# Optimization experiments

Hardware: AMD Instinct MI355X
Metric: run time of the kernel (lower is better)

Reference implementation:

```python
import jax, jax.numpy as jnp
import numpy as np

SAMPLES = 1024
LAM = 0.00051
IOR = 1.515
T_PROP = 8.74
CA = 0.9
LENSLET_CA = 0.165
RMIN = 5.5 * (IOR - 1.0)
RMAX = 29.0 * (IOR - 1.0)
NZ = 10
NLENS = 29
TAU = 30.0
LSE_P = 0.01
PS = 3.6 / SAMPLES
K = 2.0 * np.pi / LAM


def _grids():
    xg = np.linspace(-1.8, 1.8, SAMPLES).astype(np.float32)
    xgm, ygm = np.meshgrid(xg, xg)
    fx = np.linspace(-1.0 / (2.0 * PS), 1.0 / (2.0 * PS), SAMPLES).astype(np.float32)
    Fx, Fy = np.meshgrid(fx, fx)
    return xgm, ygm, Fx, Fy


def _bessj1(x):
    # Numerical Recipes rational approximation of J1 (numpy, setup-time only)
    ax = np.abs(x)
    y = x * x
    p1 = x * (72362614232.0 + y * (-7895059235.0 + y * (242396853.1 + y * (-2972611.439 + y * (15704.48260 + y * (-30.16036606))))))
    q1 = 144725228442.0 + y * (2300535178.0 + y * (18583304.74 + y * (99447.43394 + y * (376.9991397 + y))))
    small = p1 / q1
    axs = np.maximum(ax, 1e-12)
    z = 8.0 / axs
    y2 = z * z
    xx = axs - 2.356194491
    p2 = 1.0 + y2 * (0.183105e-2 + y2 * (-0.3516396496e-4 + y2 * (0.2457520174e-5 + y2 * (-0.240337019e-6))))
    q2 = 0.04687499995 + y2 * (-0.2002690873e-3 + y2 * (0.8449199096e-5 + y2 * (-0.88228987e-6 + y2 * 0.105787412e-6)))
    big = np.sqrt(0.636619772 / axs) * (np.cos(xx) * p2 - z * np.sin(xx) * q2) * np.sign(x)
    return np.where(ax < 8.0, small, big)


def _target_and_mask():
    xgm, ygm, _, _ = _grids()
    target_res = 0.005 * 6  # target_res * M
    D = 1.22 * LAM / np.sin(2.0 * np.arctan(target_res / (2.0 * T_PROP)))
    xa = K * D * np.sin(np.arctan(xgm / T_PROP)) / 2.0
    ya = K * D * np.sin(np.arctan(ygm / T_PROP)) / 2.0
    Ra = np.sqrt(xa * xa + ya * ya)
    ta = (2.0 * _bessj1(Ra) / Ra) ** 2
    ta = ta / np.sqrt(np.sum(ta ** 2))
    tF = np.abs(np.fft.fft2(np.fft.fftshift(ta))) ** 2
    dcm = np.ones_like(tF)
    dcm[:3, :3] = 0; dcm[-2:, :1] = 0; dcm[:1, -2:] = 0; dcm[-2:, -2:] = 0
    dc_mask = ((dcm * tF) > 1e-3 * tF.max()).astype(np.float32)
    return tF.astype(np.float32), dc_mask


def setup_inputs() -> dict:
    rng = np.random.default_rng(0)
    rlist = rng.permutation(1.0 / np.linspace(1.0 / RMAX, 1.0 / RMIN, NLENS)).astype(np.float32)
    th = rng.uniform(0.0, 2.0 * np.pi, NLENS)
    rad = (CA - LENSLET_CA) * np.sqrt(rng.uniform(0.0, 1.0, NLENS))
    xpos = (rad * np.cos(th)).astype(np.float32)
    ypos = (rad * np.sin(th)).astype(np.float32)
    zmin_v = 1.0 / (1.0 / T_PROP - 1.0 / 5.5)
    zmax_v = 1.0 / (1.0 / T_PROP - 1.0 / 29.0)
    defocus = (1.0 / np.linspace(1.0 / zmin_v, 1.0 / zmax_v, NZ)).astype(np.float32)
    tF, dc_mask = _target_and_mask()
    return {
        'rlist': jnp.asarray(rlist), 'xpos': jnp.asarray(xpos), 'ypos': jnp.asarray(ypos),
        'defocus_list': jnp.asarray(defocus),
        'target_F': jnp.asarray(tF), 'dc_mask': jnp.asarray(dc_mask),
    }


def reference(rlist, xpos, ypos, defocus_list, target_F, dc_mask):
    xgm_np, ygm_np, Fx_np, Fy_np = _grids()
    xgm, ygm = jnp.asarray(xgm_np), jnp.asarray(ygm_np)
    Fx, Fy = jnp.asarray(Fx_np), jnp.asarray(Fy_np)

    # ---- lenslet surface synthesis (irregular per-lenslet scatter) ----
    dx2 = (xgm[None] - xpos[:, None, None]) ** 2 + (ygm[None] - ypos[:, None, None]) ** 2  # [N,H,W]
    in_lens = dx2 <= LENSLET_CA ** 2
    r = rlist[:, None, None]
    r2_safe = jnp.where(in_lens, dx2, 0.0)  # avoid nan grads outside lenslet
    sag = r - jnp.sqrt(jnp.maximum(r * r - r2_safe, 1e-12))  # plano-convex sag
    Tsurf = jnp.sum(jnp.where(in_lens, sag, 0.0), axis=0)  # [H,W]
    aper = ((jnp.sum(in_lens.astype(jnp.float32), axis=0) > 0) & (xgm ** 2 + ygm ** 2 <= CA ** 2)).astype(jnp.float32)
    phi_lens = (K * (IOR - 1.0)) * Tsurf

    # ---- angular-spectrum propagation kernel over distance t ----
    kz = jnp.sqrt(jnp.maximum((1.0 / LAM) ** 2 - Fx ** 2 - Fy ** 2, 0.0))
    H = jnp.fft.ifftshift(jnp.exp(1j * (2.0 * np.pi * T_PROP) * kz))

    def psf_one(z):
        phi_in = K * (xgm ** 2 + ygm ** 2) / (2.0 * z)  # paraxial defocus from virtual plane z
        U1 = aper * jnp.exp(1j * (phi_in + phi_lens))
        U2 = jnp.fft.ifft2(jnp.fft.fft2(U1) * H)
        p = jnp.abs(U2) ** 2
        return p / jnp.sum(p)  # l1 psf normalization

    zstack = jax.vmap(psf_one)(defocus_list)  # [Nz,H,W]

    # ---- stack spectrum ----
    S = jnp.fft.fft2(jnp.fft.fftshift(zstack, axes=(-2, -1)))  # [Nz,H,W] complex
    normsize = float(SAMPLES * SAMPLES)

    # diagonal terms: |S|^2 vs target autocorrelation spectrum, dc-masked
    diag = jnp.sum(dc_mask[None] * jnp.square((jnp.abs(S) ** 2 - target_F[None]) / normsize), axis=(-2, -1))  # [Nz]

    # off-diagonal terms: log-sum-exp of |cross-correlation|
    i1, i2 = np.triu_indices(NZ, k=1)  # 45 fixed pairs
    Fcorr = jnp.conj(S[i1]) * S[i2]  # [45,H,W]
    ccorr = jnp.abs(jnp.fft.ifft2(Fcorr))
    off = (TAU * LSE_P) * jax.scipy.special.logsumexp(ccorr.reshape(len(i1), -1) / LSE_P, axis=-1)  # [45]

    return jnp.concatenate([diag, off], axis=0)  # [55]
```

## Files before the change

### kernel.cpp

```cpp
#include <hip/hip_runtime.h>
#include <math.h>

#define NSMP 1024
#define NZ 10
#define NLENS 29
#define NPAIR 45
#define NUNIT 23
#define UBATCH 4
#define CPB 4
#define CSTR 1028

static __device__ __forceinline__ float2 cmulf(float2 a, float2 b){
    return make_float2(a.x*b.x - a.y*b.y, a.x*b.y + a.y*b.x);
}
#define SW(i) ((i) ^ (((i)>>5)&31))

static constexpr double PI2   = 6.283185307179586;
static constexpr double KD    = PI2/0.00051;
static constexpr double F0D   = 1.0/(2.0*(3.6/1024.0));
static constexpr double FSTEP = 2.0*F0D/1023.0;
static constexpr double IL2D  = (1.0/0.00051)*(1.0/0.00051);
static constexpr double TPPID = PI2*8.74;

static __device__ __forceinline__ void fill_W(float2* W, int tid, int nthr){
    for (int t = tid; t < 1024; t += nthr){
        float a = (float)((double)t * (-PI2/1024.0));
        float s, c; sincosf(a, &s, &c);
        W[SW(t)] = make_float2(c, s);
    }
}

template<bool INV>
static __device__ __forceinline__ void bf4(const float2 a[4], float2 w1, float2 w2, float2 w3, float2 o[4]){
    if (INV){ w1.y = -w1.y; w2.y = -w2.y; w3.y = -w3.y; }
    float2 a1 = cmulf(a[1], w1), a2 = cmulf(a[2], w2), a3 = cmulf(a[3], w3);
    float2 t0 = make_float2(a[0].x+a2.x, a[0].y+a2.y);
    float2 t1 = make_float2(a[0].x-a2.x, a[0].y-a2.y);
    float2 t2 = make_float2(a1.x+a3.x, a1.y+a3.y);
    float2 t3 = make_float2(a1.x-a3.x, a1.y-a3.y);
    o[0] = make_float2(t0.x+t2.x, t0.y+t2.y);
    o[2] = make_float2(t0.x-t2.x, t0.y-t2.y);
    if (!INV){
        o[1] = make_float2(t1.x + t3.y, t1.y - t3.x);
        o[3] = make_float2(t1.x - t3.y, t1.y + t3.x);
    } else {
        o[1] = make_float2(t1.x - t3.y, t1.y + t3.x);
        o[3] = make_float2(t1.x + t3.y, t1.y - t3.x);
    }
}
template<bool INV>
static __device__ __forceinline__ void bf4nt(const float2 a[4], float2 o[4]){
    float2 t0 = make_float2(a[0].x+a[2].x, a[0].y+a[2].y);
    float2 t1 = make_float2(a[0].x-a[2].x, a[0].y-a[2].y);
    float2 t2 = make_float2(a[1].x+a[3].x, a[1].y+a[3].y);
    float2 t3 = make_float2(a[1].x-a[3].x, a[1].y-a[3].y);
    o[0] = make_float2(t0.x+t2.x, t0.y+t2.y);
    o[2] = make_float2(t0.x-t2.x, t0.y-t2.y);
    if (!INV){
        o[1] = make_float2(t1.x + t3.y, t1.y - t3.x);
        o[3] = make_float2(t1.x - t3.y, t1.y + t3.x);
    } else {
        o[1] = make_float2(t1.x - t3.y, t1.y + t3.x);
        o[3] = make_float2(t1.x + t3.y, t1.y - t3.x);
    }
}

static __device__ __forceinline__ void r16_load(const float2* B, int t, float2 a[4][4]){
    #pragma unroll
    for (int k = 0; k < 4; ++k)
        #pragma unroll
        for (int q = 0; q < 4; ++q)
            a[k][q] = B[SW(t + 64*k + 256*q)];
}
template<bool INV>
static __device__ __forceinline__ void r16_s14(const float2 a[4][4], const float2* W, float2 z[4][4]){
    float2 y[4][4];
    #pragma unroll
    for (int k = 0; k < 4; ++k) bf4nt<INV>(a[k], y[k]);
    #pragma unroll
    for (int i = 0; i < 4; ++i){
        float2 b[4] = { y[0][i], y[1][i], y[2][i], y[3][i] };
        bf4<INV>(b, W[SW(64*i)], W[SW(128*i)], W[SW(192*i)], z[i]);
    }
}
static __device__ __forceinline__ void r16_st1(float2* B, int t, const float2 z[4][4]){
    #pragma unroll
    for (int i = 0; i < 4; ++i)
        #pragma unroll
        for (int d = 0; d < 4; ++d)
            B[SW(16*t + i + 4*d)] = z[i][d];
}
template<bool INV>
static __device__ __forceinline__ void r16_s16_64(const float2 a[4][4], const float2* W, int t, float2 z[4][4]){
    int mt = t & 15;
    float2 y[4][4];
    float2 w1 = W[SW(16*mt)], w2 = W[SW(32*mt)], w3 = W[SW(48*mt)];
    #pragma unroll
    for (int k = 0; k < 4; ++k) bf4<INV>(a[k], w1, w2, w3, y[k]);
    #pragma unroll
    for (int n = 0; n < 4; ++n){
        int m2 = mt + 16*n;
        float2 b[4] = { y[0][n], y[1][n], y[2][n], y[3][n] };
        bf4<INV>(b, W[SW(4*m2)], W[SW(8*m2)], W[SW(12*m2)], z[n]);
    }
}
static __device__ __forceinline__ void r16_st2(float2* B, int t, const float2 z[4][4]){
    int base = 256*(t>>4) + (t&15);
    #pragma unroll
    for (int n = 0; n < 4; ++n)
        #pragma unroll
        for (int d = 0; d < 4; ++d)
            B[SW(base + 16*n + 64*d)] = z[n][d];
}
template<bool INV>
static __device__ __forceinline__ void r16_s256(const float2 a[4][4], const float2* W, int t, float2 z[4][4]){
    #pragma unroll
    for (int k = 0; k < 4; ++k){
        int j = t + 64*k;
        bf4<INV>(a[k], W[SW(j)], W[SW(2*j)], W[SW(3*j)], z[k]);
    }
}
static __device__ __forceinline__ void r16_st3(float2* B, int t, const float2 z[4][4]){
    #pragma unroll
    for (int k = 0; k < 4; ++k)
        #pragma unroll
        for (int d = 0; d < 4; ++d)
            B[SW(t + 64*k + 256*d)] = z[k][d];
}
template<bool INV>
static __device__ void r16_fft(float2* B, const float2* W, int t, float2 z[4][4]){
    float2 a[4][4];
    r16_load(B, t, a); r16_s14<INV>(a, W, z);
    __syncthreads(); r16_st1(B, t, z); __syncthreads();
    r16_load(B, t, a); r16_s16_64<INV>(a, W, t, z);
    __syncthreads(); r16_st2(B, t, z); __syncthreads();
    r16_load(B, t, a); r16_s256<INV>(a, W, t, z);
}

template<bool INV, int TPF>
static __device__ void fft1024_lds(float2* buf, const float2* W, int tid){
    const int WPT = 256/TPF;
    int Ns = 1;
    #pragma unroll
    for (int stage = 0; stage < 5; ++stage){
        float2 v[WPT][4];
        #pragma unroll
        for (int w = 0; w < WPT; ++w){
            int j = tid + w*TPF;
            float2 a[4] = { buf[SW(j)], buf[SW(j+256)], buf[SW(j+512)], buf[SW(j+768)] };
            int m  = j & (Ns-1);
            int tb = m * (256/Ns);
            bf4<INV>(a, W[SW(tb)], W[SW(2*tb)], W[SW(3*tb)], v[w]);
        }
        __syncthreads();
        #pragma unroll
        for (int w = 0; w < WPT; ++w){
            int j = tid + w*TPF;
            int m = j & (Ns-1);
            int idxD = ((j - m) << 2) + m;
            buf[SW(idxD)]      = v[w][0];
            buf[SW(idxD+Ns)]   = v[w][1];
            buf[SW(idxD+2*Ns)] = v[w][2];
            buf[SW(idxD+3*Ns)] = v[w][3];
        }
        __syncthreads();
        Ns <<= 2;
    }
}

static __device__ __forceinline__ float2 expi_from_double(double ph){
    double t = ph * (1.0/PI2);
    t -= floor(t);
    float th = (float)(t * PI2);
    float s, c; sincosf(th, &s, &c);
    return make_float2(c, s);
}

__global__ __launch_bounds__(256) void k_lens(const float* __restrict__ rlist,
        const float* __restrict__ xpos, const float* __restrict__ ypos,
        float2* __restrict__ phiA){
    int idx = blockIdx.x*256 + threadIdx.x;
    int r = idx >> 10, c = idx & 1023;
    float x = (float)(-1.8 + c*(3.6/1023.0));
    float y = (float)(-1.8 + r*(3.6/1023.0));
    const float ca2 = (float)(0.165*0.165);
    float T = 0.f; int any = 0;
    for (int l = 0; l < NLENS; ++l){
        float dx = x - xpos[l], dy = y - ypos[l];
        float d2 = dx*dx + dy*dy;
        if (d2 <= ca2){
            float rr = rlist[l];
            T += rr - sqrtf(fmaxf(rr*rr - d2, 1e-12f));
            any = 1;
        }
    }
    float ap = (any && (x*x + y*y) <= 0.81f) ? 1.f : 0.f;
    float phi = (float)(KD*(1.515 - 1.0)) * T;
    phiA[idx] = make_float2(phi, ap);
}

__global__ __launch_bounds__(256) void k_prep_h(float2* __restrict__ HT){
    int idx = blockIdx.x*256 + threadIdx.x;
    int c = idx >> 10, r = idx & 1023;
    int cs = (c + 512) & 1023, rs = (r + 512) & 1023;
    float fc = (float)(-F0D + cs*FSTEP);
    float fr = (float)(-F0D + rs*FSTEP);
    float kz2 = __fsub_rn(__fsub_rn((float)IL2D, __fmul_rn(fc,fc)), __fmul_rn(fr,fr));
    float kzf = sqrtf(fmaxf(kz2, 0.f));
    float phf = __fmul_rn((float)TPPID, kzf);
    HT[idx] = expi_from_double((double)phf);
}

__global__ void k_prep_tm(const float* __restrict__ tF, const float* __restrict__ dm,
                          float2* __restrict__ TM){
    __shared__ float2 T[32][33];
    int bx = blockIdx.x, by = blockIdx.y;
    int tx = threadIdx.x, ty = threadIdx.y;
    #pragma unroll
    for (int j = 0; j < 4; ++j){
        int r = by*32 + ty + 8*j, c = bx*32 + tx;
        T[ty+8*j][tx] = make_float2(tF[(size_t)r*1024 + c], dm[(size_t)r*1024 + c]);
    }
    __syncthreads();
    #pragma unroll
    for (int j = 0; j < 4; ++j){
        int c = bx*32 + ty + 8*j, r = by*32 + tx;
        TM[(size_t)c*1024 + r] = T[tx][ty+8*j];
    }
}

__global__ __launch_bounds__(256) void k_p1(const float2* __restrict__ phiA,
        const float* __restrict__ defocus, float2* __restrict__ S){
    __shared__ float2 buf[1024];
    __shared__ float2 W[1024];
    int row = blockIdx.x, z = blockIdx.y, tid = threadIdx.x;
    fill_W(W, tid, 256);
    float zf = defocus[z];
    float y  = (float)(-1.8 + row*(3.6/1023.0));
    const float KF = (float)KD;
    const float2* pha = phiA + ((size_t)row << 10);
    for (int k = 0; k < 4; ++k){
        int c = tid + k*256;
        float x = (float)(-1.8 + c*(3.6/1023.0));
        float2 pa = pha[c];
        float2 u  = make_float2(0.f, 0.f);
        if (pa.y != 0.f){
            float q      = x*x + y*y;
            float phi_in = (KF*q) / (2.0f*zf);
            u = expi_from_double((double)(phi_in + pa.x));
        }
        buf[SW(c)] = u;
    }
    __syncthreads();
    fft1024_lds<false,256>(buf, W, tid);
    float2* Srow = S + ((size_t)z << 20) + ((size_t)row << 10);
    for (int k = 0; k < 4; ++k){ int c = tid + k*256; Srow[c] = buf[SW(c)]; }
}

__global__ __launch_bounds__(256) void k_p2(float2* __restrict__ S, const float2* __restrict__ HT){
    __shared__ float2 buf[CPB*CSTR];
    __shared__ float2 W[1024];
    int tid = threadIdx.x, bx = blockIdx.x, zz = blockIdx.y;
    int cb = ((bx & 7) << 5) | (bx >> 3);
    int c0 = cb*CPB;
    fill_W(W, tid, 256);
    float2* Sz = S + ((size_t)zz << 20);
    for (int it = 0; it < 16; ++it){
        int rr = it*64 + (tid>>2), cc = tid & 3;
        buf[cc*CSTR + SW(rr)] = Sz[((size_t)rr << 10) + c0 + cc];
    }
    __syncthreads();
    int col = tid >> 6, t = tid & 63;
    float2* B = buf + col*CSTR;
    float2 a[4][4], z[4][4];
    r16_load(B, t, a); r16_s14<false>(a, W, z);
    __syncthreads(); r16_st1(B, t, z); __syncthreads();
    r16_load(B, t, a); r16_s16_64<false>(a, W, t, z);
    __syncthreads(); r16_st2(B, t, z); __syncthreads();
    r16_load(B, t, a); r16_s256<false>(a, W, t, z);
    const float2* Hc = HT + ((size_t)(c0+col) << 10);
    #pragma unroll
    for (int k = 0; k < 4; ++k)
        #pragma unroll
        for (int d = 0; d < 4; ++d)
            z[k][d] = cmulf(z[k][d], Hc[t + 64*k + 256*d]);
    r16_s14<true>(z, W, a);
    __syncthreads(); r16_st1(B, t, a); __syncthreads();
    r16_load(B, t, a); r16_s16_64<true>(a, W, t, z);
    __syncthreads(); r16_st2(B, t, z); __syncthreads();
    r16_load(B, t, a); r16_s256<true>(a, W, t, z);
    const float sc = 1.0f/1024.0f;
    #pragma unroll
    for (int k = 0; k < 4; ++k)
        #pragma unroll
        for (int d = 0; d < 4; ++d){ z[k][d].x *= sc; z[k][d].y *= sc; }
    __syncthreads();
    r16_st3(B, t, z);
    __syncthreads();
    for (int it = 0; it < 16; ++it){
        int rr = it*64 + (tid>>2), cc = tid & 3;
        Sz[((size_t)rr << 10) + c0 + cc] = buf[cc*CSTR + SW(rr)];
    }
}

__global__ __launch_bounds__(256) void k_p3(float2* __restrict__ S, float* __restrict__ sumPart){
    __shared__ float2 buf[1024];
    __shared__ float2 W[1024];
    __shared__ float red[4];
    int row = blockIdx.x, z = blockIdx.y, tid = threadIdx.x;
    fill_W(W, tid, 256);
    float2* Srow = S + ((size_t)z << 20) + ((size_t)row << 10);
    for (int k = 0; k < 4; ++k){ int c = tid + k*256; buf[SW(c)] = Srow[c]; }
    __syncthreads();
    fft1024_lds<true,256>(buf, W, tid);
    const float s2 = (1.0f/1024.0f)*(1.0f/1024.0f);
    float pv[4]; float lsum = 0.f;
    for (int k = 0; k < 4; ++k){
        int c = tid + k*256;
        float2 u = buf[SW(c)];
        float p  = (u.x*u.x + u.y*u.y) * s2;
        pv[k] = p; lsum += p;
    }
    for (int k = 0; k < 4; ++k){ int c = tid + k*256; buf[SW(c)] = make_float2(pv[k], 0.f); }
    for (int o = 32; o > 0; o >>= 1) lsum += __shfl_down(lsum, o, 64);
    if ((tid & 63) == 0) red[tid >> 6] = lsum;
    __syncthreads();
    if (tid == 0) sumPart[z*1024 + row] = red[0]+red[1]+red[2]+red[3];
    fft1024_lds<false,256>(buf, W, tid);
    for (int k = 0; k < 4; ++k){ int c = tid + k*256; Srow[c] = buf[SW(c)]; }
}

__global__ __launch_bounds__(256) void k_r1(const float* __restrict__ sumPart, double* __restrict__ sums){
    __shared__ double dred[4];
    int z = blockIdx.x, tid = threadIdx.x;
    double s = 0.0;
    for (int i = tid; i < 1024; i += 256) s += (double)sumPart[z*1024 + i];
    for (int o = 32; o > 0; o >>= 1) s += __shfl_down(s, o, 64);
    if ((tid & 63) == 0) dred[tid >> 6] = s;
    __syncthreads();
    if (tid == 0) sums[z] = dred[0]+dred[1]+dred[2]+dred[3];
}

__global__ __launch_bounds__(256) void k_p4(float2* __restrict__ S, const double* __restrict__ sums,
        const float2* __restrict__ TM, float* __restrict__ dpart){
    __shared__ float2 buf[CPB*CSTR];
    __shared__ float2 W[1024];
    __shared__ float red[4];
    int tid = threadIdx.x, bx = blockIdx.x, zz = blockIdx.y;
    int cb = ((bx & 7) << 5) | (bx >> 3);
    int c0 = cb*CPB;
    fill_W(W, tid, 256);
    float2* Sz = S + ((size_t)zz << 20);
    for (int it = 0; it < 16; ++it){
        int rr = it*64 + (tid>>2), cc = tid & 3;
        buf[cc*CSTR + SW(rr)] = Sz[((size_t)rr << 10) + c0 + cc];
    }
    __syncthreads();
    int col = tid >> 6, t = tid & 63;
    float2* B = buf + col*CSTR;
    float2 z[4][4];
    r16_fft<false>(B, W, t, z);
    float inv = (float)(1.0/sums[zz]);
    const float2* TMc = TM + ((size_t)(c0+col) << 10);
    const float nrm = 1.0f/1048576.0f;
    float dacc = 0.f;
    #pragma unroll
    for (int k = 0; k < 4; ++k)
        #pragma unroll
        for (int d = 0; d < 4; ++d){
            float2 s = z[k][d]; s.x *= inv; s.y *= inv; z[k][d] = s;
            float2 tm = TMc[t + 64*k + 256*d];
            float dff = (s.x*s.x + s.y*s.y - tm.x) * nrm;
            dacc += tm.y * dff * dff;
        }
    __syncthreads();
    r16_st3(B, t, z);
    __syncthreads();
    for (int it = 0; it < 16; ++it){
        int rr = it*64 + (tid>>2), cc = tid & 3;
        Sz[((size_t)rr << 10) + c0 + cc] = buf[cc*CSTR + SW(rr)];
    }
    for (int o = 32; o > 0; o >>= 1) dacc += __shfl_down(dacc, o, 64);
    if ((tid & 63) == 0) red[tid >> 6] = dacc;
    __syncthreads();
    if (tid == 0) dpart[zz*256 + cb] = red[0]+red[1]+red[2]+red[3];
}

static __device__ __forceinline__ void pair_of(int p, int& a, int& b){
    int i = 0, c = NZ-1;
    while (p >= c){ p -= c; ++i; --c; }
    a = i; b = i + 1 + p;
}

__global__ __launch_bounds__(256) void k_pairA(const float2* __restrict__ S,
        float2* __restrict__ U, int ubase){
    __shared__ float2 buf[1024];
    __shared__ float2 W[1024];
    int row = blockIdx.x, ug = blockIdx.y, tid = threadIdx.x;
    int u = ubase + ug;
    int pa = 2*u, pb = (2*u+1 < NPAIR) ? (2*u+1) : (NPAIR-1);
    int i1, i2, j1, j2;
    pair_of(pa, i1, i2); pair_of(pb, j1, j2);
    const float2* A1 = S + ((size_t)i1 << 20) + ((size_t)row << 10);
    const float2* A2 = S + ((size_t)i2 << 20) + ((size_t)row << 10);
    const float2* B1 = S + ((size_t)j1 << 20) + ((size_t)row << 10);
    const float2* B2 = S + ((size_t)j2 << 20) + ((size_t)row << 10);
    fill_W(W, tid, 256);
    for (int k = 0; k < 4; ++k){
        int c = tid + k*256;
        float2 x1 = A1[c], y1 = A2[c], x2 = B1[c], y2 = B2[c];
        float2 g1 = make_float2(x1.x*y1.x + x1.y*y1.y, x1.x*y1.y - x1.y*y1.x);
        float2 g2 = make_float2(x2.x*y2.x + x2.y*y2.y, x2.x*y2.y - x2.y*y2.x);
        buf[SW(c)] = make_float2(g1.x - g2.y, g1.y + g2.x);
    }
    __syncthreads();
    fft1024_lds<true,256>(buf, W, tid);
    const float sc = 1.0f/1024.0f;
    float2* Up = U + ((size_t)ug << 20) + ((size_t)row << 10);
    for (int k = 0; k < 4; ++k){
        int c = tid + k*256;
        float2 v = buf[SW(c)];
        Up[c] = make_float2(v.x*sc, v.y*sc);
    }
}

__global__ __launch_bounds__(256) void k_pairB(const float2* __restrict__ U,
        float2* __restrict__ lsePart, int ubase){
    __shared__ float2 buf[CPB*CSTR];
    __shared__ float2 W[1024];
    __shared__ float2 redA[4], redB[4];
    int tid = threadIdx.x, bx = blockIdx.x, ug = blockIdx.y;
    int cb = ((bx & 7) << 5) | (bx >> 3);
    int c0 = cb*CPB;
    int u = ubase + ug;
    fill_W(W, tid, 256);
    const float2* Up = U + ((size_t)ug << 20);
    for (int it = 0; it < 16; ++it){
        int rr = it*64 + (tid>>2), cc = tid & 3;
        buf[cc*CSTR + SW(rr)] = Up[((size_t)rr << 10) + c0 + cc];
    }
    __syncthreads();
    int col = tid >> 6, t = tid & 63;
    float2* B = buf + col*CSTR;
    float2 z[4][4];
    r16_fft<true>(B, W, t, z);
    const float sc = 1.0f/1024.0f;
    float m1 = -1.f, m2 = -1.f;
    #pragma unroll
    for (int k = 0; k < 4; ++k)
        #pragma unroll
        for (int d = 0; d < 4; ++d){
            float c1 = fabsf(z[k][d].x)*sc, c2 = fabsf(z[k][d].y)*sc;
            z[k][d] = make_float2(c1, c2);
            m1 = fmaxf(m1, c1); m2 = fmaxf(m2, c2);
        }
    for (int o = 32; o > 0; o >>= 1){
        m1 = fmaxf(m1, __shfl_down(m1, o, 64));
        m2 = fmaxf(m2, __shfl_down(m2, o, 64));
    }
    if ((tid & 63) == 0) redA[tid >> 6] = make_float2(m1, m2);
    __syncthreads();
    float M1 = fmaxf(fmaxf(redA[0].x, redA[1].x), fmaxf(redA[2].x, redA[3].x));
    float M2 = fmaxf(fmaxf(redA[0].y, redA[1].y), fmaxf(redA[2].y, redA[3].y));
    float s1 = 0.f, s2 = 0.f;
    #pragma unroll
    for (int k = 0; k < 4; ++k)
        #pragma unroll
        for (int d = 0; d < 4; ++d){
            s1 += expf((z[k][d].x - M1) * 100.0f);
            s2 += expf((z[k][d].y - M2) * 100.0f);
        }
    for (int o = 32; o > 0; o >>= 1){
        s1 += __shfl_down(s1, o, 64);
        s2 += __shfl_down(s2, o, 64);
    }
    if ((tid & 63) == 0) redB[tid >> 6] = make_float2(s1, s2);
    __syncthreads();
    if (tid == 0){
        lsePart[(size_t)(2*u)*256 + cb] = make_float2(M1, redB[0].x+redB[1].x+redB[2].x+redB[3].x);
        if (2*u+1 < NPAIR)
            lsePart[(size_t)(2*u+1)*256 + cb] = make_float2(M2, redB[0].y+redB[1].y+redB[2].y+redB[3].y);
    }
}

__global__ __launch_bounds__(256) void k_final(const float* __restrict__ dpart,
        const float2* __restrict__ lsePart, float* __restrict__ out){
    __shared__ double dred[4];
    __shared__ float fred[4];
    int b = blockIdx.x, tid = threadIdx.x;
    if (b < NZ){
        double s = (double)dpart[b*256 + tid];
        for (int o = 32; o > 0; o >>= 1) s += __shfl_down(s, o, 64);
        if ((tid & 63) == 0) dred[tid >> 6] = s;
        __syncthreads();
        if (tid == 0) out[b] = (float)(dred[0]+dred[1]+dred[2]+dred[3]);
    } else {
        int p = b - NZ;
        float2 v = lsePart[(size_t)p*256 + tid];
        float m = v.x;
        for (int o = 32; o > 0; o >>= 1) m = fmaxf(m, __shfl_down(m, o, 64));
        if ((tid & 63) == 0) fred[tid >> 6] = m;
        __syncthreads();
        float M = fmaxf(fmaxf(fred[0], fred[1]), fmaxf(fred[2], fred[3]));
        double s = (double)v.y * (double)expf((v.x - M)*100.0f);
        for (int o = 32; o > 0; o >>= 1) s += __shfl_down(s, o, 64);
        if ((tid & 63) == 0) dred[tid >> 6] = s;
        __syncthreads();
        if (tid == 0)
            out[NZ + p] = (float)(30.0*(double)M + 0.3*log(dred[0]+dred[1]+dred[2]+dred[3]));
    }
}

extern "C" void kernel_launch(void* const* d_in, const int* in_sizes, int n_in,
                              void* d_out, int out_size, void* d_ws, size_t ws_size,
                              hipStream_t stream){
    const float* rlist   = (const float*)d_in[0];
    const float* xpos    = (const float*)d_in[1];
    const float* ypos    = (const float*)d_in[2];
    const float* defocus = (const float*)d_in[3];
    const float* tF      = (const float*)d_in[4];
    const float* dmask   = (const float*)d_in[5];
    float* out = (float*)d_out;

    char* ws = (char*)d_ws;
    float2* S       = (float2*)(ws);
    char*   X       = ws + 83886080;
    float2* phiA    = (float2*)(X);
    float2* HT      = (float2*)(X + 8388608);
    float2* TM      = (float2*)(X + 16777216);
    float2* U       = (float2*)(X);
    char*   tail    = ws + 125829120;
    float*  sumPart = (float*) (tail);
    double* sums    = (double*)(tail + 65536);
    float*  dpart   = (float*) (tail + 66560);
    float2* lsePart = (float2*)(tail + 81920);

    k_lens   <<<4096, 256, 0, stream>>>(rlist, xpos, ypos, phiA);
    k_prep_h <<<4096, 256, 0, stream>>>(HT);
    k_prep_tm<<<dim3(32,32), dim3(32,8), 0, stream>>>(tF, dmask, TM);
    k_p1 <<<dim3(1024, NZ), 256, 0, stream>>>(phiA, defocus, S);
    k_p2 <<<dim3(256,  NZ), 256, 0, stream>>>(S, HT);
    k_p3 <<<dim3(1024, NZ), 256, 0, stream>>>(S, sumPart);
    k_r1 <<<NZ, 256, 0, stream>>>(sumPart, sums);
    k_p4 <<<dim3(256,  NZ), 256, 0, stream>>>(S, sums, TM, dpart);
    for (int g = 0; g < NUNIT; g += UBATCH){
        int cnt = (NUNIT - g < UBATCH) ? (NUNIT - g) : UBATCH;
        k_pairA<<<dim3(1024, cnt), 256, 0, stream>>>(S, U, g);
        k_pairB<<<dim3(256,  cnt), 256, 0, stream>>>(U, lsePart, g);
    }
    k_final<<<NZ + NPAIR, 256, 0, stream>>>(dpart, lsePart, out);
}
```

Before: 504.0 us.

## Use one wavefront per FFT row, fuse prep kernels, precompute twiddle table

Row FFT kernels (p1, p3, pairA) now give each 64-lane wavefront its own row, with data held in registers. Exchanges go through per-wave LDS using wave barriers instead of block-wide syncthreads, and each block handles 4 rows. The three setup kernels plus twiddle generation are merged into one launch, and twiddles are loaded from a global table instead of recomputed with sincos in every block. The k_r1 reduction is folded into k_p4, and the pair batch size grows to 8 when the workspace allows, which cuts launches. This adds more LDS per block (four 8 KB buffers), which may lower occupancy, and relies on the workspace being large enough for the bigger U buffer.

```diff
diff --git a/kernel.cpp b/kernel.cpp
--- a/kernel.cpp
+++ b/kernel.cpp
@@ -1,19 +1,16 @@
 #include <hip/hip_runtime.h>
 #include <math.h>
 
-#define NSMP 1024
 #define NZ 10
 #define NLENS 29
 #define NPAIR 45
 #define NUNIT 23
-#define UBATCH 4
-#define CPB 4
-#define CSTR 1028
 
 static __device__ __forceinline__ float2 cmulf(float2 a, float2 b){
     return make_float2(a.x*b.x - a.y*b.y, a.x*b.y + a.y*b.x);
 }
 #define SW(i) ((i) ^ (((i)>>5)&31))
+#define WB() __builtin_amdgcn_wave_barrier()
 
 static constexpr double PI2   = 6.283185307179586;
 static constexpr double KD    = PI2/0.00051;
@@ -22,12 +19,8 @@
 static constexpr double IL2D  = (1.0/0.00051)*(1.0/0.00051);
 static constexpr double TPPID = PI2*8.74;
 
-static __device__ __forceinline__ void fill_W(float2* W, int tid, int nthr){
-    for (int t = tid; t < 1024; t += nthr){
-        float a = (float)((double)t * (-PI2/1024.0));
-        float s, c; sincosf(a, &s, &c);
-        W[SW(t)] = make_float2(c, s);
-    }
+static __device__ __forceinline__ void load_W(float2* W, const float2* Wg, int tid){
+    for (int t = tid; t < 1024; t += 256) W[SW(t)] = Wg[t];
 }
 
 template<bool INV>
@@ -128,44 +121,19 @@
             B[SW(t + 64*k + 256*d)] = z[k][d];
 }
 template<bool INV>
-static __device__ void r16_fft(float2* B, const float2* W, int t, float2 z[4][4]){
+static __device__ void r16_fft_regs(float2* B, const float2* W, int t, float2 a[4][4], float2 z[4][4]){
+    float2 b[4][4];
+    r16_s14<INV>(a, W, z);
+    WB(); r16_st1(B, t, z); WB();
+    r16_load(B, t, b); r16_s16_64<INV>(b, W, t, z);
+    WB(); r16_st2(B, t, z); WB();
+    r16_load(B, t, b); r16_s256<INV>(b, W, t, z);
+}
+template<bool INV>
+static __device__ void r16_fft_lds(float2* B, const float2* W, int t, float2 z[4][4]){
     float2 a[4][4];
-    r16_load(B, t, a); r16_s14<INV>(a, W, z);
-    __syncthreads(); r16_st1(B, t, z); __syncthreads();
-    r16_load(B, t, a); r16_s16_64<INV>(a, W, t, z);
-    __syncthreads(); r16_st2(B, t, z); __syncthreads();
-    r16_load(B, t, a); r16_s256<INV>(a, W, t, z);
-}
-
-template<bool INV, int TPF>
-static __device__ void fft1024_lds(float2* buf, const float2* W, int tid){
-    const int WPT = 256/TPF;
-    int Ns = 1;
-    #pragma unroll
-    for (int stage = 0; stage < 5; ++stage){
-        float2 v[WPT][4];
-        #pragma unroll
-        for (int w = 0; w < WPT; ++w){
-            int j = tid + w*TPF;
-            float2 a[4] = { buf[SW(j)], buf[SW(j+256)], buf[SW(j+512)], buf[SW(j+768)] };
-            int m  = j & (Ns-1);
-            int tb = m * (256/Ns);
-            bf4<INV>(a, W[SW(tb)], W[SW(2*tb)], W[SW(3*tb)], v[w]);
-        }
-        __syncthreads();
-        #pragma unroll
-        for (int w = 0; w < WPT; ++w){
-            int j = tid + w*TPF;
-            int m = j & (Ns-1);
-            int idxD = ((j - m) << 2) + m;
-            buf[SW(idxD)]      = v[w][0];
-            buf[SW(idxD+Ns)]   = v[w][1];
-            buf[SW(idxD+2*Ns)] = v[w][2];
-            buf[SW(idxD+3*Ns)] = v[w][3];
-        }
-        __syncthreads();
-        Ns <<= 2;
-    }
+    r16_load(B, t, a);
+    r16_fft_regs<INV>(B, W, t, a, z);
 }
 
 static __device__ __forceinline__ float2 expi_from_double(double ph){
@@ -176,191 +144,208 @@
     return make_float2(c, s);
 }
 
-__global__ __launch_bounds__(256) void k_lens(const float* __restrict__ rlist,
+__global__ __launch_bounds__(256) void k_prep(const float* __restrict__ rlist,
         const float* __restrict__ xpos, const float* __restrict__ ypos,
-        float2* __restrict__ phiA){
-    int idx = blockIdx.x*256 + threadIdx.x;
-    int r = idx >> 10, c = idx & 1023;
-    float x = (float)(-1.8 + c*(3.6/1023.0));
-    float y = (float)(-1.8 + r*(3.6/1023.0));
-    const float ca2 = (float)(0.165*0.165);
-    float T = 0.f; int any = 0;
-    for (int l = 0; l < NLENS; ++l){
-        float dx = x - xpos[l], dy = y - ypos[l];
-        float d2 = dx*dx + dy*dy;
-        if (d2 <= ca2){
-            float rr = rlist[l];
-            T += rr - sqrtf(fmaxf(rr*rr - d2, 1e-12f));
-            any = 1;
-        }
-    }
-    float ap = (any && (x*x + y*y) <= 0.81f) ? 1.f : 0.f;
-    float phi = (float)(KD*(1.515 - 1.0)) * T;
-    phiA[idx] = make_float2(phi, ap);
-}
-
-__global__ __launch_bounds__(256) void k_prep_h(float2* __restrict__ HT){
-    int idx = blockIdx.x*256 + threadIdx.x;
-    int c = idx >> 10, r = idx & 1023;
-    int cs = (c + 512) & 1023, rs = (r + 512) & 1023;
-    float fc = (float)(-F0D + cs*FSTEP);
-    float fr = (float)(-F0D + rs*FSTEP);
-    float kz2 = __fsub_rn(__fsub_rn((float)IL2D, __fmul_rn(fc,fc)), __fmul_rn(fr,fr));
-    float kzf = sqrtf(fmaxf(kz2, 0.f));
-    float phf = __fmul_rn((float)TPPID, kzf);
-    HT[idx] = expi_from_double((double)phf);
-}
-
-__global__ void k_prep_tm(const float* __restrict__ tF, const float* __restrict__ dm,
-                          float2* __restrict__ TM){
+        const float* __restrict__ tF, const float* __restrict__ dm,
+        float2* __restrict__ phiA, float2* __restrict__ HT,
+        float2* __restrict__ TM, float2* __restrict__ Wg){
     __shared__ float2 T[32][33];
-    int bx = blockIdx.x, by = blockIdx.y;
-    int tx = threadIdx.x, ty = threadIdx.y;
-    #pragma unroll
-    for (int j = 0; j < 4; ++j){
-        int r = by*32 + ty + 8*j, c = bx*32 + tx;
-        T[ty+8*j][tx] = make_float2(tF[(size_t)r*1024 + c], dm[(size_t)r*1024 + c]);
-    }
-    __syncthreads();
-    #pragma unroll
-    for (int j = 0; j < 4; ++j){
-        int c = bx*32 + ty + 8*j, r = by*32 + tx;
-        TM[(size_t)c*1024 + r] = T[tx][ty+8*j];
+    int b = blockIdx.x, tid = threadIdx.x;
+    if (b < 4096){
+        int idx = b*256 + tid;
+        int r = idx >> 10, c = idx & 1023;
+        float x = (float)(-1.8 + c*(3.6/1023.0));
+        float y = (float)(-1.8 + r*(3.6/1023.0));
+        const float ca2 = (float)(0.165*0.165);
+        float Ts = 0.f; int any = 0;
+        for (int l = 0; l < NLENS; ++l){
+            float dx = x - xpos[l], dy = y - ypos[l];
+            float d2 = dx*dx + dy*dy;
+            if (d2 <= ca2){
+                float rr = rlist[l];
+                Ts += rr - sqrtf(fmaxf(rr*rr - d2, 1e-12f));
+                any = 1;
+            }
+        }
+        float ap = (any && (x*x + y*y) <= 0.81f) ? 1.f : 0.f;
+        float phi = (float)(KD*(1.515 - 1.0)) * Ts;
+        phiA[idx] = make_float2(phi, ap);
+    } else if (b < 8192){
+        int idx = (b-4096)*256 + tid;
+        int c = idx >> 10, r = idx & 1023;
+        int cs = (c + 512) & 1023, rs = (r + 512) & 1023;
+        float fc = (float)(-F0D + cs*FSTEP);
+        float fr = (float)(-F0D + rs*FSTEP);
+        float kz2 = __fsub_rn(__fsub_rn((float)IL2D, __fmul_rn(fc,fc)), __fmul_rn(fr,fr));
+        float kzf = sqrtf(fmaxf(kz2, 0.f));
+        float phf = __fmul_rn((float)TPPID, kzf);
+        HT[idx] = expi_from_double((double)phf);
+    } else if (b < 9216){
+        int tb = b - 8192;
+        int bx = tb & 31, by = tb >> 5;
+        int tx = tid & 31, ty = tid >> 5;
+        #pragma unroll
+        for (int j = 0; j < 4; ++j){
+            int r = by*32 + ty + 8*j, c = bx*32 + tx;
+            T[ty+8*j][tx] = make_float2(tF[(size_t)r*1024 + c], dm[(size_t)r*1024 + c]);
+        }
+        __syncthreads();
+        #pragma unroll
+        for (int j = 0; j < 4; ++j){
+            int c = bx*32 + ty + 8*j, r = by*32 + tx;
+            TM[(size_t)c*1024 + r] = T[tx][ty+8*j];
+        }
+    } else {
+        int t = (b-9216)*256 + tid;
+        float a = (float)((double)t * (-PI2/1024.0));
+        float s, c; sincosf(a, &s, &c);
+        Wg[t] = make_float2(c, s);
     }
 }
 
 __global__ __launch_bounds__(256) void k_p1(const float2* __restrict__ phiA,
-        const float* __restrict__ defocus, float2* __restrict__ S){
-    __shared__ float2 buf[1024];
+        const float* __restrict__ defocus, float2* __restrict__ S,
+        const float2* __restrict__ Wg){
+    __shared__ float2 buf[4*1024];
     __shared__ float2 W[1024];
-    int row = blockIdx.x, z = blockIdx.y, tid = threadIdx.x;
-    fill_W(W, tid, 256);
-    float zf = defocus[z];
+    int tid = threadIdx.x, zz = blockIdx.y;
+    load_W(W, Wg, tid);
+    __syncthreads();
+    int w = tid >> 6, t = tid & 63;
+    int row = blockIdx.x*4 + w;
+    float2* B = buf + w*1024;
+    float zf = defocus[zz];
     float y  = (float)(-1.8 + row*(3.6/1023.0));
     const float KF = (float)KD;
     const float2* pha = phiA + ((size_t)row << 10);
-    for (int k = 0; k < 4; ++k){
-        int c = tid + k*256;
-        float x = (float)(-1.8 + c*(3.6/1023.0));
-        float2 pa = pha[c];
-        float2 u  = make_float2(0.f, 0.f);
-        if (pa.y != 0.f){
-            float q      = x*x + y*y;
-            float phi_in = (KF*q) / (2.0f*zf);
-            u = expi_from_double((double)(phi_in + pa.x));
-        }
-        buf[SW(c)] = u;
-    }
-    __syncthreads();
-    fft1024_lds<false,256>(buf, W, tid);
-    float2* Srow = S + ((size_t)z << 20) + ((size_t)row << 10);
-    for (int k = 0; k < 4; ++k){ int c = tid + k*256; Srow[c] = buf[SW(c)]; }
-}
-
-__global__ __launch_bounds__(256) void k_p2(float2* __restrict__ S, const float2* __restrict__ HT){
-    __shared__ float2 buf[CPB*CSTR];
+    float2 a[4][4], z[4][4];
+    #pragma unroll
+    for (int k = 0; k < 4; ++k)
+        #pragma unroll
+        for (int q = 0; q < 4; ++q){
+            int idx = t + 64*k + 256*q;
+            float x = (float)(-1.8 + idx*(3.6/1023.0));
+            float2 pa = pha[idx];
+            float2 u  = make_float2(0.f, 0.f);
+            if (pa.y != 0.f){
+                float qq     = x*x + y*y;
+                float phi_in = (KF*qq) / (2.0f*zf);
+                u = expi_from_double((double)(phi_in + pa.x));
+            }
+            a[k][q] = u;
+        }
+    r16_fft_regs<false>(B, W, t, a, z);
+    float2* Srow = S + ((size_t)zz << 20) + ((size_t)row << 10);
+    #pragma unroll
+    for (int k = 0; k < 4; ++k)
+        #pragma unroll
+        for (int d = 0; d < 4; ++d)
+            Srow[t + 64*k + 256*d] = z[k][d];
+}
+
+__global__ __launch_bounds__(256) void k_p2(float2* __restrict__ S,
+        const float2* __restrict__ HT, const float2* __restrict__ Wg){
+    __shared__ float2 buf[4*1024];
     __shared__ float2 W[1024];
     int tid = threadIdx.x, bx = blockIdx.x, zz = blockIdx.y;
     int cb = ((bx & 7) << 5) | (bx >> 3);
-    int c0 = cb*CPB;
-    fill_W(W, tid, 256);
+    int c0 = cb*4;
+    load_W(W, Wg, tid);
     float2* Sz = S + ((size_t)zz << 20);
     for (int it = 0; it < 16; ++it){
         int rr = it*64 + (tid>>2), cc = tid & 3;
-        buf[cc*CSTR + SW(rr)] = Sz[((size_t)rr << 10) + c0 + cc];
+        buf[cc*1024 + SW(rr)] = Sz[((size_t)rr << 10) + c0 + cc];
     }
     __syncthreads();
     int col = tid >> 6, t = tid & 63;
-    float2* B = buf + col*CSTR;
-    float2 a[4][4], z[4][4];
-    r16_load(B, t, a); r16_s14<false>(a, W, z);
-    __syncthreads(); r16_st1(B, t, z); __syncthreads();
-    r16_load(B, t, a); r16_s16_64<false>(a, W, t, z);
-    __syncthreads(); r16_st2(B, t, z); __syncthreads();
-    r16_load(B, t, a); r16_s256<false>(a, W, t, z);
+    float2* B = buf + col*1024;
+    float2 z[4][4], a[4][4];
+    r16_fft_lds<false>(B, W, t, z);
     const float2* Hc = HT + ((size_t)(c0+col) << 10);
     #pragma unroll
     for (int k = 0; k < 4; ++k)
         #pragma unroll
         for (int d = 0; d < 4; ++d)
             z[k][d] = cmulf(z[k][d], Hc[t + 64*k + 256*d]);
-    r16_s14<true>(z, W, a);
-    __syncthreads(); r16_st1(B, t, a); __syncthreads();
-    r16_load(B, t, a); r16_s16_64<true>(a, W, t, z);
-    __syncthreads(); r16_st2(B, t, z); __syncthreads();
-    r16_load(B, t, a); r16_s256<true>(a, W, t, z);
+    r16_fft_regs<true>(B, W, t, z, a);
     const float sc = 1.0f/1024.0f;
     #pragma unroll
     for (int k = 0; k < 4; ++k)
         #pragma unroll
-        for (int d = 0; d < 4; ++d){ z[k][d].x *= sc; z[k][d].y *= sc; }
-    __syncthreads();
-    r16_st3(B, t, z);
+        for (int d = 0; d < 4; ++d){ a[k][d].x *= sc; a[k][d].y *= sc; }
+    WB();
+    r16_st3(B, t, a);
     __syncthreads();
     for (int it = 0; it < 16; ++it){
         int rr = it*64 + (tid>>2), cc = tid & 3;
-        Sz[((size_t)rr << 10) + c0 + cc] = buf[cc*CSTR + SW(rr)];
-    }
-}
-
-__global__ __launch_bounds__(256) void k_p3(float2* __restrict__ S, float* __restrict__ sumPart){
-    __shared__ float2 buf[1024];
+        Sz[((size_t)rr << 10) + c0 + cc] = buf[cc*1024 + SW(rr)];
+    }
+}
+
+__global__ __launch_bounds__(256) void k_p3(float2* __restrict__ S,
+        float* __restrict__ sumPart, const float2* __restrict__ Wg){
+    __shared__ float2 buf[4*1024];
     __shared__ float2 W[1024];
-    __shared__ float red[4];
-    int row = blockIdx.x, z = blockIdx.y, tid = threadIdx.x;
-    fill_W(W, tid, 256);
-    float2* Srow = S + ((size_t)z << 20) + ((size_t)row << 10);
-    for (int k = 0; k < 4; ++k){ int c = tid + k*256; buf[SW(c)] = Srow[c]; }
-    __syncthreads();
-    fft1024_lds<true,256>(buf, W, tid);
+    int tid = threadIdx.x, zz = blockIdx.y;
+    load_W(W, Wg, tid);
+    __syncthreads();
+    int w = tid >> 6, t = tid & 63;
+    int row = blockIdx.x*4 + w;
+    float2* B = buf + w*1024;
+    float2* Srow = S + ((size_t)zz << 20) + ((size_t)row << 10);
+    float2 a[4][4], z[4][4];
+    #pragma unroll
+    for (int k = 0; k < 4; ++k)
+        #pragma unroll
+        for (int q = 0; q < 4; ++q)
+            a[k][q] = Srow[t + 64*k + 256*q];
+    r16_fft_regs<true>(B, W, t, a, z);
     const float s2 = (1.0f/1024.0f)*(1.0f/1024.0f);
-    float pv[4]; float lsum = 0.f;
-    for (int k = 0; k < 4; ++k){
-        int c = tid + k*256;
-        float2 u = buf[SW(c)];
-        float p  = (u.x*u.x + u.y*u.y) * s2;
-        pv[k] = p; lsum += p;
-    }
-    for (int k = 0; k < 4; ++k){ int c = tid + k*256; buf[SW(c)] = make_float2(pv[k], 0.f); }
+    float lsum = 0.f;
+    #pragma unroll
+    for (int k = 0; k < 4; ++k)
+        #pragma unroll
+        for (int d = 0; d < 4; ++d){
+            float2 u = z[k][d];
+            float p = (u.x*u.x + u.y*u.y) * s2;
+            a[k][d] = make_float2(p, 0.f);
+            lsum += p;
+        }
     for (int o = 32; o > 0; o >>= 1) lsum += __shfl_down(lsum, o, 64);
-    if ((tid & 63) == 0) red[tid >> 6] = lsum;
-    __syncthreads();
-    if (tid == 0) sumPart[z*1024 + row] = red[0]+red[1]+red[2]+red[3];
-    fft1024_lds<false,256>(buf, W, tid);
-    for (int k = 0; k < 4; ++k){ int c = tid + k*256; Srow[c] = buf[SW(c)]; }
-}
-
-__global__ __launch_bounds__(256) void k_r1(const float* __restrict__ sumPart, double* __restrict__ sums){
-    __shared__ double dred[4];
-    int z = blockIdx.x, tid = threadIdx.x;
-    double s = 0.0;
-    for (int i = tid; i < 1024; i += 256) s += (double)sumPart[z*1024 + i];
-    for (int o = 32; o > 0; o >>= 1) s += __shfl_down(s, o, 64);
-    if ((tid & 63) == 0) dred[tid >> 6] = s;
-    __syncthreads();
-    if (tid == 0) sums[z] = dred[0]+dred[1]+dred[2]+dred[3];
-}
-
-__global__ __launch_bounds__(256) void k_p4(float2* __restrict__ S, const double* __restrict__ sums,
-        const float2* __restrict__ TM, float* __restrict__ dpart){
-    __shared__ float2 buf[CPB*CSTR];
+    if (t == 0) sumPart[zz*1024 + row] = lsum;
+    WB();
+    r16_fft_regs<false>(B, W, t, a, z);
+    #pragma unroll
+    for (int k = 0; k < 4; ++k)
+        #pragma unroll
+        for (int d = 0; d < 4; ++d)
+            Srow[t + 64*k + 256*d] = z[k][d];
+}
+
+__global__ __launch_bounds__(256) void k_p4(float2* __restrict__ S,
+        const float* __restrict__ sumPart, const float2* __restrict__ TM,
+        float* __restrict__ dpart, const float2* __restrict__ Wg){
+    __shared__ float2 buf[4*1024];
     __shared__ float2 W[1024];
-    __shared__ float red[4];
     int tid = threadIdx.x, bx = blockIdx.x, zz = blockIdx.y;
     int cb = ((bx & 7) << 5) | (bx >> 3);
-    int c0 = cb*CPB;
-    fill_W(W, tid, 256);
+    int c0 = cb*4;
+    load_W(W, Wg, tid);
     float2* Sz = S + ((size_t)zz << 20);
     for (int it = 0; it < 16; ++it){
         int rr = it*64 + (tid>>2), cc = tid & 3;
-        buf[cc*CSTR + SW(rr)] = Sz[((size_t)rr << 10) + c0 + cc];
-    }
-    __syncthreads();
+        buf[cc*1024 + SW(rr)] = Sz[((size_t)rr << 10) + c0 + cc];
+    }
     int col = tid >> 6, t = tid & 63;
-    float2* B = buf + col*CSTR;
+    double sd = 0.0;
+    for (int i = t; i < 1024; i += 64) sd += (double)sumPart[zz*1024 + i];
+    for (int o = 32; o > 0; o >>= 1) sd += __shfl_down(sd, o, 64);
+    sd = __shfl(sd, 0, 64);
+    float inv = (float)(1.0/sd);
+    __syncthreads();
+    float2* B = buf + col*1024;
     float2 z[4][4];
-    r16_fft<false>(B, W, t, z);
-    float inv = (float)(1.0/sums[zz]);
+    r16_fft_lds<false>(B, W, t, z);
     const float2* TMc = TM + ((size_t)(c0+col) << 10);
     const float nrm = 1.0f/1048576.0f;
     float dacc = 0.f;
@@ -373,17 +358,20 @@
             float dff = (s.x*s.x + s.y*s.y - tm.x) * nrm;
             dacc += tm.y * dff * dff;
         }
-    __syncthreads();
+    for (int o = 32; o > 0; o >>= 1) dacc += __shfl_down(dacc, o, 64);
+    WB();
     r16_st3(B, t, z);
     __syncthreads();
+    if (t == 0) ((float*)W)[col] = dacc;
     for (int it = 0; it < 16; ++it){
         int rr = it*64 + (tid>>2), cc = tid & 3;
-        Sz[((size_t)rr << 10) + c0 + cc] = buf[cc*CSTR + SW(rr)];
-    }
-    for (int o = 32; o > 0; o >>= 1) dacc += __shfl_down(dacc, o, 64);
-    if ((tid & 63) == 0) red[tid >> 6] = dacc;
-    __syncthreads();
-    if (tid == 0) dpart[zz*256 + cb] = red[0]+red[1]+red[2]+red[3];
+        Sz[((size_t)rr << 10) + c0 + cc] = buf[cc*1024 + SW(rr)];
+    }
+    __syncthreads();
+    if (tid == 0){
+        float* r = (float*)W;
+        dpart[zz*256 + cb] = r[0]+r[1]+r[2]+r[3];
+    }
 }
 
 static __device__ __forceinline__ void pair_of(int p, int& a, int& b){
@@ -393,10 +381,15 @@
 }
 
 __global__ __launch_bounds__(256) void k_pairA(const float2* __restrict__ S,
-        float2* __restrict__ U, int ubase){
-    __shared__ float2 buf[1024];
+        float2* __restrict__ U, int ubase, const float2* __restrict__ Wg){
+    __shared__ float2 buf[4*1024];
     __shared__ float2 W[1024];
-    int row = blockIdx.x, ug = blockIdx.y, tid = threadIdx.x;
+    int tid = threadIdx.x, ug = blockIdx.y;
+    load_W(W, Wg, tid);
+    __syncthreads();
+    int w = tid >> 6, t = tid & 63;
+    int row = blockIdx.x*4 + w;
+    float2* B = buf + w*1024;
     int u = ubase + ug;
     int pa = 2*u, pb = (2*u+1 < NPAIR) ? (2*u+1) : (NPAIR-1);
     int i1, i2, j1, j2;
@@ -405,45 +398,48 @@
     const float2* A2 = S + ((size_t)i2 << 20) + ((size_t)row << 10);
     const float2* B1 = S + ((size_t)j1 << 20) + ((size_t)row << 10);
     const float2* B2 = S + ((size_t)j2 << 20) + ((size_t)row << 10);
-    fill_W(W, tid, 256);
-    for (int k = 0; k < 4; ++k){
-        int c = tid + k*256;
-        float2 x1 = A1[c], y1 = A2[c], x2 = B1[c], y2 = B2[c];
-        float2 g1 = make_float2(x1.x*y1.x + x1.y*y1.y, x1.x*y1.y - x1.y*y1.x);
-        float2 g2 = make_float2(x2.x*y2.x + x2.y*y2.y, x2.x*y2.y - x2.y*y2.x);
-        buf[SW(c)] = make_float2(g1.x - g2.y, g1.y + g2.x);
-    }
-    __syncthreads();
-    fft1024_lds<true,256>(buf, W, tid);
+    float2 a[4][4], z[4][4];
+    #pragma unroll
+    for (int k = 0; k < 4; ++k)
+        #pragma unroll
+        for (int q = 0; q < 4; ++q){
+            int idx = t + 64*k + 256*q;
+            float2 x1 = A1[idx], y1 = A2[idx], x2 = B1[idx], y2 = B2[idx];
+            float2 g1 = make_float2(x1.x*y1.x + x1.y*y1.y, x1.x*y1.y - x1.y*y1.x);
+            float2 g2 = make_float2(x2.x*y2.x + x2.y*y2.y, x2.x*y2.y - x2.y*y2.x);
+            a[k][q] = make_float2(g1.x - g2.y, g1.y + g2.x);
+        }
+    r16_fft_regs<true>(B, W, t, a, z);
     const float sc = 1.0f/1024.0f;
     float2* Up = U + ((size_t)ug << 20) + ((size_t)row << 10);
-    for (int k = 0; k < 4; ++k){
-        int c = tid + k*256;
-        float2 v = buf[SW(c)];
-        Up[c] = make_float2(v.x*sc, v.y*sc);
-    }
+    #pragma unroll
+    for (int k = 0; k < 4; ++k)
+        #pragma unroll
+        for (int d = 0; d < 4; ++d){
+            float2 v = z[k][d];
+            Up[t + 64*k + 256*d] = make_float2(v.x*sc, v.y*sc);
+        }
 }
 
 __global__ __launch_bounds__(256) void k_pairB(const float2* __restrict__ U,
-        float2* __restrict__ lsePart, int ubase){
-    __shared__ float2 buf[CPB*CSTR];
+        float2* __restrict__ lsePart, int ubase, const float2* __restrict__ Wg){
+    __shared__ float2 buf[4*1024];
     __shared__ float2 W[1024];
-    __shared__ float2 redA[4], redB[4];
     int tid = threadIdx.x, bx = blockIdx.x, ug = blockIdx.y;
     int cb = ((bx & 7) << 5) | (bx >> 3);
-    int c0 = cb*CPB;
+    int c0 = cb*4;
     int u = ubase + ug;
-    fill_W(W, tid, 256);
+    load_W(W, Wg, tid);
     const float2* Up = U + ((size_t)ug << 20);
     for (int it = 0; it < 16; ++it){
         int rr = it*64 + (tid>>2), cc = tid & 3;
-        buf[cc*CSTR + SW(rr)] = Up[((size_t)rr << 10) + c0 + cc];
+        buf[cc*1024 + SW(rr)] = Up[((size_t)rr << 10) + c0 + cc];
     }
     __syncthreads();
     int col = tid >> 6, t = tid & 63;
-    float2* B = buf + col*CSTR;
+    float2* B = buf + col*1024;
     float2 z[4][4];
-    r16_fft<true>(B, W, t, z);
+    r16_fft_lds<true>(B, W, t, z);
     const float sc = 1.0f/1024.0f;
     float m1 = -1.f, m2 = -1.f;
     #pragma unroll
@@ -458,10 +454,14 @@
         m1 = fmaxf(m1, __shfl_down(m1, o, 64));
         m2 = fmaxf(m2, __shfl_down(m2, o, 64));
     }
-    if ((tid & 63) == 0) redA[tid >> 6] = make_float2(m1, m2);
-    __syncthreads();
-    float M1 = fmaxf(fmaxf(redA[0].x, redA[1].x), fmaxf(redA[2].x, redA[3].x));
-    float M2 = fmaxf(fmaxf(redA[0].y, redA[1].y), fmaxf(redA[2].y, redA[3].y));
+    if (t == 0) B[0] = make_float2(m1, m2);
+    __syncthreads();
+    float M1 = -1.f, M2 = -1.f;
+    #pragma unroll
+    for (int ww = 0; ww < 4; ++ww){
+        float2 v = buf[ww*1024];
+        M1 = fmaxf(M1, v.x); M2 = fmaxf(M2, v.y);
+    }
     float s1 = 0.f, s2 = 0.f;
     #pragma unroll
     for (int k = 0; k < 4; ++k)
@@ -474,12 +474,18 @@
         s1 += __shfl_down(s1, o, 64);
         s2 += __shfl_down(s2, o, 64);
     }
-    if ((tid & 63) == 0) redB[tid >> 6] = make_float2(s1, s2);
+    if (t == 0) B[1] = make_float2(s1, s2);
     __syncthreads();
     if (tid == 0){
-        lsePart[(size_t)(2*u)*256 + cb] = make_float2(M1, redB[0].x+redB[1].x+redB[2].x+redB[3].x);
+        float S1 = 0.f, S2 = 0.f;
+        #pragma unroll
+        for (int ww = 0; ww < 4; ++ww){
+            float2 v = buf[ww*1024 + 1];
+            S1 += v.x; S2 += v.y;
+        }
+        lsePart[(size_t)(2*u)*256 + cb] = make_float2(M1, S1);
         if (2*u+1 < NPAIR)
-            lsePart[(size_t)(2*u+1)*256 + cb] = make_float2(M2, redB[0].y+redB[1].y+redB[2].y+redB[3].y);
+            lsePart[(size_t)(2*u+1)*256 + cb] = make_float2(M2, S2);
     }
 }
 
@@ -523,30 +529,31 @@
     float* out = (float*)d_out;
 
     char* ws = (char*)d_ws;
+    const size_t S_B = 83886080ull;
     float2* S       = (float2*)(ws);
-    char*   X       = ws + 83886080;
+    char*   tail    = ws + S_B;
+    float*  sumPart = (float*) (tail);
+    float*  dpart   = (float*) (tail + 65536);
+    float2* lsePart = (float2*)(tail + 131072);
+    float2* Wg      = (float2*)(tail + 229376);
+    char*   X       = ws + S_B + 262144;
     float2* phiA    = (float2*)(X);
     float2* HT      = (float2*)(X + 8388608);
     float2* TM      = (float2*)(X + 16777216);
     float2* U       = (float2*)(X);
-    char*   tail    = ws + 125829120;
-    float*  sumPart = (float*) (tail);
-    double* sums    = (double*)(tail + 65536);
-    float*  dpart   = (float*) (tail + 66560);
-    float2* lsePart = (float2*)(tail + 81920);
-
-    k_lens   <<<4096, 256, 0, stream>>>(rlist, xpos, ypos, phiA);
-    k_prep_h <<<4096, 256, 0, stream>>>(HT);
-    k_prep_tm<<<dim3(32,32), dim3(32,8), 0, stream>>>(tF, dmask, TM);
-    k_p1 <<<dim3(1024, NZ), 256, 0, stream>>>(phiA, defocus, S);
-    k_p2 <<<dim3(256,  NZ), 256, 0, stream>>>(S, HT);
-    k_p3 <<<dim3(1024, NZ), 256, 0, stream>>>(S, sumPart);
-    k_r1 <<<NZ, 256, 0, stream>>>(sumPart, sums);
-    k_p4 <<<dim3(256,  NZ), 256, 0, stream>>>(S, sums, TM, dpart);
-    for (int g = 0; g < NUNIT; g += UBATCH){
-        int cnt = (NUNIT - g < UBATCH) ? (NUNIT - g) : UBATCH;
-        k_pairA<<<dim3(1024, cnt), 256, 0, stream>>>(S, U, g);
-        k_pairB<<<dim3(256,  cnt), 256, 0, stream>>>(U, lsePart, g);
+
+    size_t Xoff = S_B + 262144;
+    int UB = (ws_size >= Xoff + (64ull<<20)) ? 8 : 6;
+
+    k_prep<<<9220, 256, 0, stream>>>(rlist, xpos, ypos, tF, dmask, phiA, HT, TM, Wg);
+    k_p1 <<<dim3(256, NZ), 256, 0, stream>>>(phiA, defocus, S, Wg);
+    k_p2 <<<dim3(256, NZ), 256, 0, stream>>>(S, HT, Wg);
+    k_p3 <<<dim3(256, NZ), 256, 0, stream>>>(S, sumPart, Wg);
+    k_p4 <<<dim3(256, NZ), 256, 0, stream>>>(S, sumPart, TM, dpart, Wg);
+    for (int g = 0; g < NUNIT; g += UB){
+        int cnt = (NUNIT - g < UB) ? (NUNIT - g) : UB;
+        k_pairA<<<dim3(256, cnt), 256, 0, stream>>>(S, U, g, Wg);
+        k_pairB<<<dim3(256, cnt), 256, 0, stream>>>(U, lsePart, g, Wg);
     }
     k_final<<<NZ + NPAIR, 256, 0, stream>>>(dpart, lsePart, out);
 }
```

Result: slower. 525.4 us (+4.2%).
